# Optimization experiments

Hardware: AMD Instinct MI355X
Metric: run time of the kernel (lower is better)

Reference implementation:

```python
import jax, jax.numpy as jnp
import numpy as np


def setup_inputs() -> dict:
    key = jax.random.key(0)
    k1, k2 = jax.random.split(key)
    B, N, M, D = 4, 8192, 8192, 3
    inp = jax.random.normal(k1, (B, N, D), dtype=jnp.float32)
    pnt = jax.random.normal(k2, (B, M, D), dtype=jnp.float32)
    return {"input": inp, "point": pnt}


def reference(input, point):
    # Per-query nearest-neighbor squared distance:
    # out[b, n] = min_m || input[b, n] - point[b, m] ||^2
    # Use ||a||^2 + ||b||^2 - 2 a.b to avoid materializing [B, N, M, D].
    sq_in = jnp.sum(input * input, axis=-1)          # [B, N]
    sq_pt = jnp.sum(point * point, axis=-1)          # [B, M]
    cross = jnp.einsum('bnd,bmd->bnm', input, point) # [B, N, M]
    d2 = sq_in[:, :, None] + sq_pt[:, None, :] - 2.0 * cross
    d2 = jnp.maximum(d2, 0.0)  # numerical guard
    return jnp.min(d2, axis=-1)  # [B, N]
```

## Files before the change

### kernel.cpp

```cpp
#include <hip/hip_runtime.h>
#include <hip/hip_bf16.h>

constexpr int B = 4;
constexpr int N = 8192;
constexpr int M = 8192;

constexpr int QT      = 32;
constexpr int WAVES   = 4;
constexpr int QB      = QT * WAVES;
constexpr int QTILES  = N / QB;
constexpr int PCHUNKS = 8;
constexpr int CHUNK   = M / PCHUNKS;
constexpr int PTILES  = CHUNK / 32;

typedef __bf16 bf16x8 __attribute__((ext_vector_type(8)));
typedef float  f32x16 __attribute__((ext_vector_type(16)));

union FragU { uint4 u; bf16x8 b; };

__device__ __host__ inline unsigned f2bf(float x) {
    unsigned u = __float_as_uint(x);
    return (u + 0x7FFFu + ((u >> 16) & 1u)) >> 16;
}
__device__ inline float bf2f(unsigned b) { return __uint_as_float(b << 16); }
__device__ inline unsigned pk(unsigned lo, unsigned hi) { return lo | (hi << 16); }


__global__ __launch_bounds__(256) void prep_kernel(const float* __restrict__ point,
                                                   uint4* __restrict__ wtab) {
    int i = blockIdx.x * 256 + threadIdx.x;
    if (i >= B * M) return;
    const float p0 = point[3 * i + 0];
    const float p1 = point[3 * i + 1];
    const float p2 = point[3 * i + 2];
    const float v0 = -2.0f * p0, v1 = -2.0f * p1, v2 = -2.0f * p2;
    const unsigned h0 = f2bf(v0), l0 = f2bf(v0 - bf2f(h0));
    const unsigned h1 = f2bf(v1), l1 = f2bf(v1 - bf2f(h1));
    const unsigned h2 = f2bf(v2), l2 = f2bf(v2 - bf2f(h2));
    const float s = fmaf(p0, p0, fmaf(p1, p1, p2 * p2));
    const unsigned sh = f2bf(s), sl = f2bf(s - bf2f(sh));
    uint4 f0, f1;
    f0.x = pk(h0, h0); f0.y = pk(l0, l0); f0.z = pk(h1, h1); f0.w = pk(l1, l1);
    f1.x = pk(h2, h2); f1.y = pk(l2, l2); f1.z = pk(sh, sl); f1.w = 0;
    wtab[2 * i + 0] = f0;
    wtab[2 * i + 1] = f1;
}

__global__ __launch_bounds__(256) void main_kernel(const float* __restrict__ input,
                                                   const uint4* __restrict__ wtab,
                                                   unsigned int* __restrict__ out) {
    const int bid    = blockIdx.x;
    const int pchunk = bid % PCHUNKS;
    const int qtile  = (bid / PCHUNKS) % QTILES;
    const int b      = bid / (PCHUNKS * QTILES);
    const int tid    = threadIdx.x;
    const int wave   = tid >> 6;
    const int lane   = tid & 63;
    const int col    = lane & 31;
    const int h      = lane >> 5;

    const int q = qtile * QB + wave * QT + col;
    const float* a = input + ((size_t)b * N + q) * 3;
    const float a0 = a[0], a1 = a[1], a2 = a[2];
    const float sq_a = fmaf(a0, a0, fmaf(a1, a1, a2 * a2));
    const unsigned ah0 = f2bf(a0), al0 = f2bf(a0 - bf2f(ah0));
    const unsigned ah1 = f2bf(a1), al1 = f2bf(a1 - bf2f(ah1));
    const unsigned ah2 = f2bf(a2), al2 = f2bf(a2 - bf2f(ah2));

    FragU bq;
    const unsigned dA = h ? pk(ah2, al2) : pk(ah0, al0);
    const unsigned dB = h ? 0x3F803F80u  : pk(ah1, al1);
    bq.u.x = dA;
    bq.u.y = dA;
    bq.u.z = dB;
    bq.u.w = h ? 0u : dB;

    const uint4* __restrict__ wp =
        wtab + ((size_t)b * M + (size_t)pchunk * CHUNK) * 2;

    f32x16 cz;
    f32x16 rmin;
#pragma unroll
    for (int i = 0; i < 16; ++i) { cz[i] = 0.0f; rmin[i] = 1e30f; }

    for (int t = 0; t < PTILES; t += 2) {
        FragU fa0, fa1;
        fa0.u = wp[((t * 32 + col) << 1) + h];
        fa1.u = wp[(((t + 1) * 32 + col) << 1) + h];
        f32x16 acc0 = __builtin_amdgcn_mfma_f32_32x32x16_bf16(fa0.b, bq.b, cz, 0, 0, 0);
        f32x16 acc1 = __builtin_amdgcn_mfma_f32_32x32x16_bf16(fa1.b, bq.b, cz, 0, 0, 0);
#pragma unroll
        for (int i = 0; i < 16; ++i)
            rmin[i] = fminf(rmin[i], fminf(acc0[i], acc1[i]));
    }

    float m = rmin[0];
#pragma unroll
    for (int i = 1; i < 16; ++i) m = fminf(m, rmin[i]);
    m = fminf(m, __shfl_xor(m, 32, 64));

    if (lane < 32) {
        const float d2 = fmaxf(m + sq_a, 0.0f);
        atomicMin(&out[(size_t)b * N + q], __float_as_uint(d2));
    }
}

extern "C" void kernel_launch(void* const* d_in, const int* in_sizes, int n_in,
                              void* d_out, int out_size, void* d_ws, size_t ws_size,
                              hipStream_t stream) {
    const float* input = (const float*)d_in[0];
    const float* point = (const float*)d_in[1];
    unsigned int* out  = (unsigned int*)d_out;

    uint4* wtab = (uint4*)d_ws;

    (void)hipMemsetAsync(d_out, 0x7F, (size_t)out_size * sizeof(float), stream);

    const int prep_grid = (B * M + 255) / 256;
    const int main_grid = B * QTILES * PCHUNKS;

    prep_kernel<<<prep_grid, 256, 0, stream>>>(point, wtab);
    main_kernel<<<main_grid, 256, 0, stream>>>(input, wtab, out);
}
```

Baseline: 73.13 us.

## Register-block two query tiles per wave and fold output init into prep kernel

Each wave now handles 64 queries as two 32-column B fragments, so every loaded point fragment feeds two MFMAs and the global loads per MFMA are halved. The point dimension is split into 16 chunks instead of 8 to keep the grid size unchanged, and launch bounds ask for 3 blocks per CU. The output memset is removed and the 0x7F7F7F7F init is written from the prep kernel, which drops one launch but relies on B*M equalling B*N. Register pressure rises with the extra accumulators and min registers.

```diff
diff --git a/kernel.cpp b/kernel.cpp
--- a/kernel.cpp
+++ b/kernel.cpp
@@ -5,11 +5,11 @@
 constexpr int N = 8192;
 constexpr int M = 8192;
 
-constexpr int QT      = 32;
+constexpr int QPW     = 64;
 constexpr int WAVES   = 4;
-constexpr int QB      = QT * WAVES;
+constexpr int QB      = QPW * WAVES;
 constexpr int QTILES  = N / QB;
-constexpr int PCHUNKS = 8;
+constexpr int PCHUNKS = 16;
 constexpr int CHUNK   = M / PCHUNKS;
 constexpr int PTILES  = CHUNK / 32;
 
@@ -27,7 +27,8 @@
 
 
 __global__ __launch_bounds__(256) void prep_kernel(const float* __restrict__ point,
-                                                   uint4* __restrict__ wtab) {
+                                                   uint4* __restrict__ wtab,
+                                                   unsigned int* __restrict__ out) {
     int i = blockIdx.x * 256 + threadIdx.x;
     if (i >= B * M) return;
     const float p0 = point[3 * i + 0];
@@ -44,11 +45,30 @@
     f1.x = pk(h2, h2); f1.y = pk(l2, l2); f1.z = pk(sh, sl); f1.w = 0;
     wtab[2 * i + 0] = f0;
     wtab[2 * i + 1] = f1;
+    out[i] = 0x7F7F7F7Fu;
 }
 
-__global__ __launch_bounds__(256) void main_kernel(const float* __restrict__ input,
-                                                   const uint4* __restrict__ wtab,
-                                                   unsigned int* __restrict__ out) {
+__device__ inline FragU make_bfrag(const float* __restrict__ input,
+                                   int b, int q, int h, float& sq_a) {
+    const float* a = input + ((size_t)b * N + q) * 3;
+    const float a0 = a[0], a1 = a[1], a2 = a[2];
+    sq_a = fmaf(a0, a0, fmaf(a1, a1, a2 * a2));
+    const unsigned ah0 = f2bf(a0), al0 = f2bf(a0 - bf2f(ah0));
+    const unsigned ah1 = f2bf(a1), al1 = f2bf(a1 - bf2f(ah1));
+    const unsigned ah2 = f2bf(a2), al2 = f2bf(a2 - bf2f(ah2));
+    FragU bq;
+    const unsigned dA = h ? pk(ah2, al2) : pk(ah0, al0);
+    const unsigned dB = h ? 0x3F803F80u  : pk(ah1, al1);
+    bq.u.x = dA;
+    bq.u.y = dA;
+    bq.u.z = dB;
+    bq.u.w = h ? 0u : dB;
+    return bq;
+}
+
+__global__ __launch_bounds__(256, 3) void main_kernel(const float* __restrict__ input,
+                                                      const uint4* __restrict__ wtab,
+                                                      unsigned int* __restrict__ out) {
     const int bid    = blockIdx.x;
     const int pchunk = bid % PCHUNKS;
     const int qtile  = (bid / PCHUNKS) % QTILES;
@@ -59,49 +79,43 @@
     const int col    = lane & 31;
     const int h      = lane >> 5;
 
-    const int q = qtile * QB + wave * QT + col;
-    const float* a = input + ((size_t)b * N + q) * 3;
-    const float a0 = a[0], a1 = a[1], a2 = a[2];
-    const float sq_a = fmaf(a0, a0, fmaf(a1, a1, a2 * a2));
-    const unsigned ah0 = f2bf(a0), al0 = f2bf(a0 - bf2f(ah0));
-    const unsigned ah1 = f2bf(a1), al1 = f2bf(a1 - bf2f(ah1));
-    const unsigned ah2 = f2bf(a2), al2 = f2bf(a2 - bf2f(ah2));
-
-    FragU bq;
-    const unsigned dA = h ? pk(ah2, al2) : pk(ah0, al0);
-    const unsigned dB = h ? 0x3F803F80u  : pk(ah1, al1);
-    bq.u.x = dA;
-    bq.u.y = dA;
-    bq.u.z = dB;
-    bq.u.w = h ? 0u : dB;
+    const int q0 = qtile * QB + wave * QPW + col;
+    const int q1 = q0 + 32;
+    float sq_a0, sq_a1;
+    const FragU b0 = make_bfrag(input, b, q0, h, sq_a0);
+    const FragU b1 = make_bfrag(input, b, q1, h, sq_a1);
 
     const uint4* __restrict__ wp =
         wtab + ((size_t)b * M + (size_t)pchunk * CHUNK) * 2;
 
-    f32x16 cz;
-    f32x16 rmin;
+    f32x16 cz, rmin0, rmin1;
 #pragma unroll
-    for (int i = 0; i < 16; ++i) { cz[i] = 0.0f; rmin[i] = 1e30f; }
+    for (int i = 0; i < 16; ++i) { cz[i] = 0.0f; rmin0[i] = 1e30f; rmin1[i] = 1e30f; }
 
     for (int t = 0; t < PTILES; t += 2) {
         FragU fa0, fa1;
         fa0.u = wp[((t * 32 + col) << 1) + h];
         fa1.u = wp[(((t + 1) * 32 + col) << 1) + h];
-        f32x16 acc0 = __builtin_amdgcn_mfma_f32_32x32x16_bf16(fa0.b, bq.b, cz, 0, 0, 0);
-        f32x16 acc1 = __builtin_amdgcn_mfma_f32_32x32x16_bf16(fa1.b, bq.b, cz, 0, 0, 0);
+        f32x16 acc00 = __builtin_amdgcn_mfma_f32_32x32x16_bf16(fa0.b, b0.b, cz, 0, 0, 0);
+        f32x16 acc01 = __builtin_amdgcn_mfma_f32_32x32x16_bf16(fa0.b, b1.b, cz, 0, 0, 0);
+        f32x16 acc10 = __builtin_amdgcn_mfma_f32_32x32x16_bf16(fa1.b, b0.b, cz, 0, 0, 0);
+        f32x16 acc11 = __builtin_amdgcn_mfma_f32_32x32x16_bf16(fa1.b, b1.b, cz, 0, 0, 0);
 #pragma unroll
-        for (int i = 0; i < 16; ++i)
-            rmin[i] = fminf(rmin[i], fminf(acc0[i], acc1[i]));
+        for (int i = 0; i < 16; ++i) {
+            rmin0[i] = fminf(rmin0[i], fminf(acc00[i], acc10[i]));
+            rmin1[i] = fminf(rmin1[i], fminf(acc01[i], acc11[i]));
+        }
     }
 
-    float m = rmin[0];
+    float m0 = rmin0[0], m1 = rmin1[0];
 #pragma unroll
-    for (int i = 1; i < 16; ++i) m = fminf(m, rmin[i]);
-    m = fminf(m, __shfl_xor(m, 32, 64));
+    for (int i = 1; i < 16; ++i) { m0 = fminf(m0, rmin0[i]); m1 = fminf(m1, rmin1[i]); }
+    m0 = fminf(m0, __shfl_xor(m0, 32, 64));
+    m1 = fminf(m1, __shfl_xor(m1, 32, 64));
 
     if (lane < 32) {
-        const float d2 = fmaxf(m + sq_a, 0.0f);
-        atomicMin(&out[(size_t)b * N + q], __float_as_uint(d2));
+        atomicMin(&out[(size_t)b * N + q0], __float_as_uint(fmaxf(m0 + sq_a0, 0.0f)));
+        atomicMin(&out[(size_t)b * N + q1], __float_as_uint(fmaxf(m1 + sq_a1, 0.0f)));
     }
 }
 
@@ -114,11 +128,9 @@
 
     uint4* wtab = (uint4*)d_ws;
 
-    (void)hipMemsetAsync(d_out, 0x7F, (size_t)out_size * sizeof(float), stream);
-
     const int prep_grid = (B * M + 255) / 256;
     const int main_grid = B * QTILES * PCHUNKS;
 
-    prep_kernel<<<prep_grid, 256, 0, stream>>>(point, wtab);
+    prep_kernel<<<prep_grid, 256, 0, stream>>>(point, wtab, out);
     main_kernel<<<main_grid, 256, 0, stream>>>(input, wtab, out);
 }
```

After: 66.52 us (median of 2 runs). -9.0%, faster.
